# Optimization experiments

Measured on AMD Instinct MI355X. Metric: run time of the kernel, lower is better.

Reference implementation:

```python
import jax, jax.numpy as jnp
import numpy as np


def _gcn_layer(x, src, dst, W, b):
    """PyG GCNConv: out = D^-1/2 (A+I) D^-1/2 (x @ W) + b, symmetric norm with self-loops."""
    n = x.shape[0]
    h = x @ W  # [n, out]
    loop = jnp.arange(n, dtype=src.dtype)
    s = jnp.concatenate([src, loop])  # self-loops appended
    d = jnp.concatenate([dst, loop])
    deg = jax.ops.segment_sum(jnp.ones_like(s, dtype=x.dtype), d, num_segments=n)
    dinv = jax.lax.rsqrt(jnp.maximum(deg, 1.0))  # deg >= 1 due to self-loops
    coef = dinv[s] * dinv[d]  # [E+n]
    agg = jax.ops.segment_sum(h[s] * coef[:, None], d, num_segments=n)  # [n, out]
    return agg + b


def setup_inputs() -> dict:
    key = jax.random.key(0)
    k = jax.random.split(key, 6)
    N, E, IN, HID, OUT = 100000, 3200000, 256, 256, 128
    x = jax.random.normal(k[0], (N, IN), dtype=jnp.float32)
    edge_index = jax.random.randint(k[1], (2, E), 0, N, dtype=jnp.int64)
    # Glorot-ish init for weights, zero bias (PyG defaults)
    W1 = jax.random.normal(k[2], (IN, HID), dtype=jnp.float32) * (1.0 / np.sqrt(IN))
    b1 = jnp.zeros((HID,), dtype=jnp.float32)
    W2 = jax.random.normal(k[3], (HID, OUT), dtype=jnp.float32) * (1.0 / np.sqrt(HID))
    b2 = jnp.zeros((OUT,), dtype=jnp.float32)
    return {"x": x, "edge_index": edge_index, "W1": W1, "b1": b1, "W2": W2, "b2": b2}


def reference(x, edge_index, W1, b1, W2, b2):
    src, dst = edge_index[0], edge_index[1]
    h = jax.nn.relu(_gcn_layer(x, src, dst, W1, b1))
    return _gcn_layer(h, src, dst, W2, b2)
```

## Files before the change

kernel.cpp:

```cpp
#include <hip/hip_runtime.h>

using f32x4 = __attribute__((ext_vector_type(4))) float;
using s16x8 = __attribute__((ext_vector_type(8))) short;

static __device__ __forceinline__ unsigned short f2bf(float f) {
    union { float f; unsigned u; } v; v.f = f;
    unsigned r = v.u + 0x7fffu + ((v.u >> 16) & 1u);
    return (unsigned short)(r >> 16);
}
static __device__ __forceinline__ float bf2f(unsigned short h) {
    union { unsigned u; float f; } v; v.u = ((unsigned)h) << 16;
    return v.f;
}


__global__ __launch_bounds__(256) void partition_edges256(
        const int* __restrict__ src, const int* __restrict__ dst,
        int2* __restrict__ qpair, int* __restrict__ qcnt,
        int E, int span2, int qcap) {
    __shared__ int2 buf[256][32];
    __shared__ int cnt[256];
    const int tid = threadIdx.x;
    cnt[tid] = 0;
    __syncthreads();

    const int e0 = blockIdx.x * 2048;
    const int e1 = min(e0 + 2048, E);
    for (int i = e0 + tid; i < e1; i += 256) {
        int d = dst[i];
        int s = src[i];
        int b = (unsigned)d / (unsigned)span2;
        int p = atomicAdd(&cnt[b], 1);
        if (p < 32) {
            buf[b][p] = make_int2(d, s);
        } else {
            int gp = atomicAdd(&qcnt[b], 1);
            qpair[(size_t)b * qcap + gp] = make_int2(d, s);
        }
    }
    __syncthreads();
    int c = min(cnt[tid], 32);
    if (c > 0) {
        int gb = atomicAdd(&qcnt[tid], c);
        int2* q = qpair + (size_t)tid * qcap + gb;
        for (int j = 0; j < c; ++j) q[j] = buf[tid][j];
    }
}


__global__ __launch_bounds__(1024) void hist_bucket(
        const int2* __restrict__ qpair, const int* __restrict__ qcnt,
        int* __restrict__ deg, int N, int span2, int qcap) {
    __shared__ int h[512];
    const int b = blockIdx.x;
    const int base = b * span2;
    for (int k = threadIdx.x; k < span2; k += 1024) h[k] = 0;
    __syncthreads();
    const int len = qcnt[b];
    const int2* q = qpair + (size_t)b * qcap;
    for (int i = threadIdx.x; i < len; i += 1024)
        atomicAdd(&h[q[i].x - base], 1);
    __syncthreads();
    int width = N - base; if (width > span2) width = span2; if (width < 0) width = 0;
    for (int k = threadIdx.x; k < width; k += 1024) deg[base + k] = h[k];
}


__global__ void scan_blocks(const int* __restrict__ deg, int* __restrict__ excl,
                            int* __restrict__ block_sums, float* __restrict__ dinv, int n) {
    __shared__ int s[256];
    int t = threadIdx.x;
    int gid = blockIdx.x * 256 + t;
    int v = (gid < n) ? deg[gid] : 0;
    if (gid < n) dinv[gid] = rsqrtf((float)(v + 1));
    s[t] = v;
    __syncthreads();
    #pragma unroll
    for (int off = 1; off < 256; off <<= 1) {
        int add = (t >= off) ? s[t - off] : 0;
        __syncthreads();
        s[t] += add;
        __syncthreads();
    }
    if (gid < n) excl[gid] = s[t] - v;
    if (t == 255) block_sums[blockIdx.x] = s[255];
}

__global__ void scan_sums(int* __restrict__ block_sums, int nb) {
    __shared__ int s[512];
    int t = threadIdx.x;
    int v = (t < nb) ? block_sums[t] : 0;
    s[t] = v;
    __syncthreads();
    #pragma unroll
    for (int off = 1; off < 512; off <<= 1) {
        int add = (t >= off) ? s[t - off] : 0;
        __syncthreads();
        s[t] += add;
        __syncthreads();
    }
    if (t < nb) block_sums[t] = s[t] - v;
}

__global__ void scan_add(int* __restrict__ excl, const int* __restrict__ block_sums,
                         int n, int E) {
    int gid = blockIdx.x * 256 + threadIdx.x;
    if (gid < n) excl[gid] += block_sums[gid >> 8];
    if (gid == n) excl[n] = E;
}


__global__ __launch_bounds__(1024) void place_bucket(
        const int2* __restrict__ qpair, const int* __restrict__ qcnt,
        const int* __restrict__ rp, int* __restrict__ sorted_src,
        int N, int span2, int qcap) {
    __shared__ int cur[512];
    const int b = blockIdx.x;
    const int base = b * span2;
    for (int k = threadIdx.x; k < span2; k += 1024) {
        int idx = base + k;
        cur[k] = (idx < N) ? rp[idx] : 0;
    }
    __syncthreads();
    const int len = qcnt[b];
    const int2* q = qpair + (size_t)b * qcap;
    for (int i = threadIdx.x; i < len; i += 1024) {
        int2 p = q[i];
        int pos = atomicAdd(&cur[p.x - base], 1);
        sorted_src[pos] = p.y;
    }
}


__global__ void convert_weights_t(const float* __restrict__ W1, const float* __restrict__ W2,
                                  unsigned short* __restrict__ W1t, unsigned short* __restrict__ W2t,
                                  int K, int N1, int N2) {
    int i = blockIdx.x * blockDim.x + threadIdx.x;
    int k4 = K / 4;
    int tot1 = N1 * k4;
    int tot2 = N2 * k4;
    if (i < tot1) {
        int n = i / k4, k0 = (i % k4) * 4;
        ushort4 o = make_ushort4(f2bf(W1[(size_t)(k0 + 0) * N1 + n]),
                                 f2bf(W1[(size_t)(k0 + 1) * N1 + n]),
                                 f2bf(W1[(size_t)(k0 + 2) * N1 + n]),
                                 f2bf(W1[(size_t)(k0 + 3) * N1 + n]));
        *(ushort4*)&W1t[(size_t)n * K + k0] = o;
    } else if (i - tot1 < tot2) {
        int j = i - tot1;
        int n = j / k4, k0 = (j % k4) * 4;
        ushort4 o = make_ushort4(f2bf(W2[(size_t)(k0 + 0) * N2 + n]),
                                 f2bf(W2[(size_t)(k0 + 1) * N2 + n]),
                                 f2bf(W2[(size_t)(k0 + 2) * N2 + n]),
                                 f2bf(W2[(size_t)(k0 + 3) * N2 + n]));
        *(ushort4*)&W2t[(size_t)n * K + k0] = o;
    }
}


template<int BN, bool AF32>
__global__ __launch_bounds__(512) void gemm_mfma(
        const void* __restrict__ Av, const unsigned short* __restrict__ Bt_g,
        unsigned short* __restrict__ C, const float* __restrict__ dinv,
        int M, int K) {
    constexpr int FN = BN / 64;
    __shared__ __align__(16) short As[128][40];
    __shared__ __align__(16) short Bt[BN][40];

    const int tid  = threadIdx.x;
    const int lane = tid & 63;
    const int wave = tid >> 6;
    const int wm = wave >> 2;
    const int wn = wave & 3;
    const int brow = blockIdx.x * 128;

    const int fr = lane & 15;
    const int kk = (lane >> 4) * 8;

    const int ar = tid >> 2;
    const int ac = (tid & 3) * 8;

    f32x4 acc[4][FN] = {};

    for (int k0 = 0; k0 < K; k0 += 32) {
        {
            int gr = brow + ar;
            s16x8 s = {};
            if (gr < M) {
                if constexpr (AF32) {
                    const float* A = (const float*)Av;
                    float4 v0 = *(const float4*)&A[(size_t)gr * K + k0 + ac];
                    float4 v1 = *(const float4*)&A[(size_t)gr * K + k0 + ac + 4];
                    s[0] = (short)f2bf(v0.x); s[1] = (short)f2bf(v0.y);
                    s[2] = (short)f2bf(v0.z); s[3] = (short)f2bf(v0.w);
                    s[4] = (short)f2bf(v1.x); s[5] = (short)f2bf(v1.y);
                    s[6] = (short)f2bf(v1.z); s[7] = (short)f2bf(v1.w);
                } else {
                    const unsigned short* A = (const unsigned short*)Av;
                    s = *(const s16x8*)&A[(size_t)gr * K + k0 + ac];
                }
            }
            *(s16x8*)&As[ar][ac] = s;
        }
        #pragma unroll
        for (int p = 0; p < BN / 128; ++p) {
            int ci = tid + p * 512;
            int col = ci >> 2;
            int kc = (ci & 3) * 8;
            s16x8 v = *(const s16x8*)&Bt_g[(size_t)col * K + k0 + kc];
            *(s16x8*)&Bt[col][kc] = v;
        }
        __syncthreads();

        s16x8 af[4], bv[FN];
        #pragma unroll
        for (int fm = 0; fm < 4; ++fm)
            af[fm] = *(const s16x8*)&As[wm * 64 + fm * 16 + fr][kk];
        #pragma unroll
        for (int fn = 0; fn < FN; ++fn)
            bv[fn] = *(const s16x8*)&Bt[wn * (BN / 4) + fn * 16 + fr][kk];
        #pragma unroll
        for (int fm = 0; fm < 4; ++fm)
            #pragma unroll
            for (int fn = 0; fn < FN; ++fn)
                acc[fm][fn] = __builtin_amdgcn_mfma_f32_16x16x32_bf16(
                    af[fm], bv[fn], acc[fm][fn], 0, 0, 0);
        __syncthreads();
    }

    const int orow = (lane >> 4) * 4;
    #pragma unroll
    for (int fm = 0; fm < 4; ++fm) {
        #pragma unroll
        for (int reg = 0; reg < 4; ++reg) {
            int gr = brow + wm * 64 + fm * 16 + orow + reg;
            if (gr < M) {
                float dv = dinv[gr];
                #pragma unroll
                for (int fn = 0; fn < FN; ++fn) {
                    int gc = wn * (BN / 4) + fn * 16 + fr;
                    C[(size_t)gr * BN + gc] = f2bf(dv * acc[fm][fn][reg]);
                }
            }
        }
    }
}


__global__ __launch_bounds__(256) void agg_pull_256_bf16(
        const int* __restrict__ rp, const int* __restrict__ sorted_src,
        const float* __restrict__ dinv, const unsigned short* __restrict__ Hs,
        const float* __restrict__ bias, unsigned short* __restrict__ outb, int N) {
    int node = blockIdx.x * 4 + (threadIdx.x >> 6);
    int lane = threadIdx.x & 63;
    if (node >= N) return;

    int r0 = rp[node];
    int r1 = rp[node + 1];
    int c = lane << 2;
    ushort4 hv = *(const ushort4*)&Hs[(size_t)node * 256 + c];
    float a0 = bf2f(hv.x), a1 = bf2f(hv.y), a2 = bf2f(hv.z), a3 = bf2f(hv.w);

    int i = r0;
    for (; i + 8 <= r1; i += 8) {
        int s[8];
        #pragma unroll
        for (int u = 0; u < 8; ++u) s[u] = sorted_src[i + u];
        ushort4 h[8];
        #pragma unroll
        for (int u = 0; u < 8; ++u) h[u] = *(const ushort4*)&Hs[(size_t)s[u] * 256 + c];
        #pragma unroll
        for (int u = 0; u < 8; ++u) {
            a0 += bf2f(h[u].x); a1 += bf2f(h[u].y);
            a2 += bf2f(h[u].z); a3 += bf2f(h[u].w);
        }
    }
    if (i + 4 <= r1) {
        int s[4];
        #pragma unroll
        for (int u = 0; u < 4; ++u) s[u] = sorted_src[i + u];
        ushort4 h[4];
        #pragma unroll
        for (int u = 0; u < 4; ++u) h[u] = *(const ushort4*)&Hs[(size_t)s[u] * 256 + c];
        #pragma unroll
        for (int u = 0; u < 4; ++u) {
            a0 += bf2f(h[u].x); a1 += bf2f(h[u].y);
            a2 += bf2f(h[u].z); a3 += bf2f(h[u].w);
        }
        i += 4;
    }
    for (; i < r1; ++i) {
        ushort4 h = *(const ushort4*)&Hs[(size_t)sorted_src[i] * 256 + c];
        a0 += bf2f(h.x); a1 += bf2f(h.y); a2 += bf2f(h.z); a3 += bf2f(h.w);
    }

    float dv = dinv[node];
    float4 bb = *(const float4*)&bias[c];
    float o0 = fmaxf(bb.x + dv * a0, 0.f);
    float o1 = fmaxf(bb.y + dv * a1, 0.f);
    float o2 = fmaxf(bb.z + dv * a2, 0.f);
    float o3 = fmaxf(bb.w + dv * a3, 0.f);
    *(ushort4*)&outb[(size_t)node * 256 + c] = make_ushort4(f2bf(o0), f2bf(o1), f2bf(o2), f2bf(o3));
}


__global__ __launch_bounds__(256) void agg_pull_128_bf16(
        const int* __restrict__ rp, const int* __restrict__ sorted_src,
        const float* __restrict__ dinv, const unsigned short* __restrict__ Hs,
        const float* __restrict__ bias, float* __restrict__ out, int N) {
    int node = blockIdx.x * 8 + ((threadIdx.x >> 6) << 1) + ((threadIdx.x >> 5) & 1);
    int l = threadIdx.x & 31;
    if (node >= N) return;

    int r0 = rp[node];
    int r1 = rp[node + 1];
    int c = l << 2;
    ushort4 hv = *(const ushort4*)&Hs[(size_t)node * 128 + c];
    float a0 = bf2f(hv.x), a1 = bf2f(hv.y), a2 = bf2f(hv.z), a3 = bf2f(hv.w);

    int i = r0;
    for (; i + 8 <= r1; i += 8) {
        int s[8];
        #pragma unroll
        for (int u = 0; u < 8; ++u) s[u] = sorted_src[i + u];
        ushort4 h[8];
        #pragma unroll
        for (int u = 0; u < 8; ++u) h[u] = *(const ushort4*)&Hs[(size_t)s[u] * 128 + c];
        #pragma unroll
        for (int u = 0; u < 8; ++u) {
            a0 += bf2f(h[u].x); a1 += bf2f(h[u].y);
            a2 += bf2f(h[u].z); a3 += bf2f(h[u].w);
        }
    }
    if (i + 4 <= r1) {
        int s[4];
        #pragma unroll
        for (int u = 0; u < 4; ++u) s[u] = sorted_src[i + u];
        ushort4 h[4];
        #pragma unroll
        for (int u = 0; u < 4; ++u) h[u] = *(const ushort4*)&Hs[(size_t)s[u] * 128 + c];
        #pragma unroll
        for (int u = 0; u < 4; ++u) {
            a0 += bf2f(h[u].x); a1 += bf2f(h[u].y);
            a2 += bf2f(h[u].z); a3 += bf2f(h[u].w);
        }
        i += 4;
    }
    for (; i < r1; ++i) {
        ushort4 h = *(const ushort4*)&Hs[(size_t)sorted_src[i] * 128 + c];
        a0 += bf2f(h.x); a1 += bf2f(h.y); a2 += bf2f(h.z); a3 += bf2f(h.w);
    }

    float dv = dinv[node];
    float4 bb = *(const float4*)&bias[c];
    float4 o = make_float4(bb.x + dv * a0, bb.y + dv * a1,
                           bb.z + dv * a2, bb.w + dv * a3);
    *(float4*)&out[(size_t)node * 128 + c] = o;
}


extern "C" void kernel_launch(void* const* d_in, const int* in_sizes, int n_in,
                              void* d_out, int out_size, void* d_ws, size_t ws_size,
                              hipStream_t stream) {
    const float* x   = (const float*)d_in[0];
    const int*   ei  = (const int*)d_in[1];
    const float* W1  = (const float*)d_in[2];
    const float* b1  = (const float*)d_in[3];
    const float* W2  = (const float*)d_in[4];
    const float* b2  = (const float*)d_in[5];
    float* out       = (float*)d_out;

    const int E   = in_sizes[1] / 2;
    const int HID = in_sizes[3];
    const int IN  = in_sizes[2] / HID;
    const int OUT = in_sizes[5];
    const int N   = in_sizes[0] / IN;
    const int span2 = (N + 255) / 256;
    const int qcap  = E / 256 + 1536;

    char* ws = (char*)d_ws;
    int*   row_ptr    = (int*)ws;
    int*   deg        = (int*)(ws + (512 << 10));
    float* dinv       = (float*)(ws + (1 << 20));
    int*   block_sums = (int*)(ws + 1572864);
    int*   qcnt       = (int*)(ws + 1638400);
    unsigned short* W1t = (unsigned short*)(ws + 1703936);
    unsigned short* W2t = (unsigned short*)(ws + 1867776);
    int*   sorted_src = (int*)(ws + (2 << 20));
    unsigned short* Hsb = (unsigned short*)(ws + ((size_t)16 << 20));
    unsigned short* A1b = (unsigned short*)(ws + ((size_t)80 << 20));
    int2*  qpair      = (int2*)(ws + ((size_t)136 << 20));

    const int* e_src = ei;
    const int* e_dst = ei + E;
    const int nb_scan = (N + 255) / 256;

    hipMemsetAsync(qcnt, 0, 256 * sizeof(int), stream);
    partition_edges256<<<(E + 2047) / 2048, 256, 0, stream>>>(e_src, e_dst, qpair, qcnt,
                                                              E, span2, qcap);
    hist_bucket<<<256, 1024, 0, stream>>>(qpair, qcnt, deg, N, span2, qcap);
    scan_blocks<<<nb_scan, 256, 0, stream>>>(deg, row_ptr, block_sums, dinv, N);
    scan_sums<<<1, 512, 0, stream>>>(block_sums, nb_scan);
    scan_add<<<(N + 256) / 256, 256, 0, stream>>>(row_ptr, block_sums, N, E);
    place_bucket<<<256, 1024, 0, stream>>>(qpair, qcnt, row_ptr, sorted_src, N, span2, qcap);

    convert_weights_t<<<96, 256, 0, stream>>>(W1, W2, W1t, W2t, IN, HID, OUT);

    gemm_mfma<256, true><<<(N + 127) / 128, 512, 0, stream>>>(x, W1t, Hsb, dinv, N, IN);
    agg_pull_256_bf16<<<(N + 3) / 4, 256, 0, stream>>>(row_ptr, sorted_src, dinv, Hsb, b1, A1b, N);

    gemm_mfma<128, false><<<(N + 127) / 128, 512, 0, stream>>>(A1b, W2t, Hsb, dinv, N, HID);
    agg_pull_128_bf16<<<(N + 7) / 8, 256, 0, stream>>>(row_ptr, sorted_src, dinv, Hsb, b2, out, N);
}
```

Baseline: 485.7 us.

## Fuse CSR build into one bucket kernel and prefetch GEMM A tiles into registers

Merges the histogram, the three-pass prefix scan and the placement kernel into a single per-bucket kernel. Each bucket finds its global edge offset by summing the earlier bucket counts and scans its own 512 node degrees locally, which removes four launches and the deg/block_sums round trips through global memory. The GEMM now loads the next K-slice of A into registers while the current slice is computed, and gets a launch-bounds occupancy hint. The in-block scan assumes span2 <= 512, and the extra prefetch registers could lower occupancy.

```diff
diff --git a/kernel.cpp b/kernel.cpp
--- a/kernel.cpp
+++ b/kernel.cpp
@@ -48,85 +48,53 @@
 }
 
 
-__global__ __launch_bounds__(1024) void hist_bucket(
+__global__ __launch_bounds__(1024) void csr_bucket(
         const int2* __restrict__ qpair, const int* __restrict__ qcnt,
-        int* __restrict__ deg, int N, int span2, int qcap) {
+        int* __restrict__ row_ptr, float* __restrict__ dinv,
+        int* __restrict__ sorted_src, int N, int E, int span2, int qcap) {
+    __shared__ int red[256];
     __shared__ int h[512];
     const int b = blockIdx.x;
     const int base = b * span2;
-    for (int k = threadIdx.x; k < span2; k += 1024) h[k] = 0;
-    __syncthreads();
+    const int tid = threadIdx.x;
+
+    if (tid < 256) red[tid] = (tid < b) ? qcnt[tid] : 0;
+    __syncthreads();
+    #pragma unroll
+    for (int off = 128; off > 0; off >>= 1) {
+        if (tid < off) red[tid] += red[tid + off];
+        __syncthreads();
+    }
+    const int qbase = red[0];
     const int len = qcnt[b];
     const int2* q = qpair + (size_t)b * qcap;
-    for (int i = threadIdx.x; i < len; i += 1024)
+
+    if (tid < 512) h[tid] = 0;
+    __syncthreads();
+    for (int i = tid; i < len; i += 1024)
         atomicAdd(&h[q[i].x - base], 1);
     __syncthreads();
-    int width = N - base; if (width > span2) width = span2; if (width < 0) width = 0;
-    for (int k = threadIdx.x; k < width; k += 1024) deg[base + k] = h[k];
-}
-
-
-__global__ void scan_blocks(const int* __restrict__ deg, int* __restrict__ excl,
-                            int* __restrict__ block_sums, float* __restrict__ dinv, int n) {
-    __shared__ int s[256];
-    int t = threadIdx.x;
-    int gid = blockIdx.x * 256 + t;
-    int v = (gid < n) ? deg[gid] : 0;
-    if (gid < n) dinv[gid] = rsqrtf((float)(v + 1));
-    s[t] = v;
-    __syncthreads();
-    #pragma unroll
-    for (int off = 1; off < 256; off <<= 1) {
-        int add = (t >= off) ? s[t - off] : 0;
-        __syncthreads();
-        s[t] += add;
-        __syncthreads();
-    }
-    if (gid < n) excl[gid] = s[t] - v;
-    if (t == 255) block_sums[blockIdx.x] = s[255];
-}
-
-__global__ void scan_sums(int* __restrict__ block_sums, int nb) {
-    __shared__ int s[512];
-    int t = threadIdx.x;
-    int v = (t < nb) ? block_sums[t] : 0;
-    s[t] = v;
-    __syncthreads();
+
+    int deg_t = (tid < 512) ? h[tid] : 0;
     #pragma unroll
     for (int off = 1; off < 512; off <<= 1) {
-        int add = (t >= off) ? s[t - off] : 0;
-        __syncthreads();
-        s[t] += add;
-        __syncthreads();
-    }
-    if (t < nb) block_sums[t] = s[t] - v;
-}
-
-__global__ void scan_add(int* __restrict__ excl, const int* __restrict__ block_sums,
-                         int n, int E) {
-    int gid = blockIdx.x * 256 + threadIdx.x;
-    if (gid < n) excl[gid] += block_sums[gid >> 8];
-    if (gid == n) excl[n] = E;
-}
-
-
-__global__ __launch_bounds__(1024) void place_bucket(
-        const int2* __restrict__ qpair, const int* __restrict__ qcnt,
-        const int* __restrict__ rp, int* __restrict__ sorted_src,
-        int N, int span2, int qcap) {
-    __shared__ int cur[512];
-    const int b = blockIdx.x;
-    const int base = b * span2;
-    for (int k = threadIdx.x; k < span2; k += 1024) {
-        int idx = base + k;
-        cur[k] = (idx < N) ? rp[idx] : 0;
-    }
-    __syncthreads();
-    const int len = qcnt[b];
-    const int2* q = qpair + (size_t)b * qcap;
-    for (int i = threadIdx.x; i < len; i += 1024) {
+        int add = (tid >= off && tid < 512) ? h[tid - off] : 0;
+        __syncthreads();
+        if (tid < 512) h[tid] += add;
+        __syncthreads();
+    }
+    int width = N - base; if (width > span2) width = span2; if (width < 0) width = 0;
+    if (tid < width) {
+        row_ptr[base + tid] = qbase + h[tid] - deg_t;
+        dinv[base + tid] = rsqrtf((float)(deg_t + 1));
+    }
+    if (b == 255 && tid == 0) row_ptr[N] = E;
+
+    if (tid < 512) h[tid] = qbase + h[tid] - deg_t;
+    __syncthreads();
+    for (int i = tid; i < len; i += 1024) {
         int2 p = q[i];
-        int pos = atomicAdd(&cur[p.x - base], 1);
+        int pos = atomicAdd(&h[p.x - base], 1);
         sorted_src[pos] = p.y;
     }
 }
@@ -159,7 +127,7 @@
 
 
 template<int BN, bool AF32>
-__global__ __launch_bounds__(512) void gemm_mfma(
+__global__ __launch_bounds__(512, 4) void gemm_mfma(
         const void* __restrict__ Av, const unsigned short* __restrict__ Bt_g,
         unsigned short* __restrict__ C, const float* __restrict__ dinv,
         int M, int K) {
@@ -179,26 +147,33 @@
 
     const int ar = tid >> 2;
     const int ac = (tid & 3) * 8;
+    const int gr = brow + ar;
 
     f32x4 acc[4][FN] = {};
+    float4 pa0 = make_float4(0.f, 0.f, 0.f, 0.f), pa1 = pa0;
+    s16x8 pas = {};
+
+    if (gr < M) {
+        if constexpr (AF32) {
+            const float* A = (const float*)Av;
+            pa0 = *(const float4*)&A[(size_t)gr * K + ac];
+            pa1 = *(const float4*)&A[(size_t)gr * K + ac + 4];
+        } else {
+            const unsigned short* A = (const unsigned short*)Av;
+            pas = *(const s16x8*)&A[(size_t)gr * K + ac];
+        }
+    }
 
     for (int k0 = 0; k0 < K; k0 += 32) {
         {
-            int gr = brow + ar;
-            s16x8 s = {};
-            if (gr < M) {
-                if constexpr (AF32) {
-                    const float* A = (const float*)Av;
-                    float4 v0 = *(const float4*)&A[(size_t)gr * K + k0 + ac];
-                    float4 v1 = *(const float4*)&A[(size_t)gr * K + k0 + ac + 4];
-                    s[0] = (short)f2bf(v0.x); s[1] = (short)f2bf(v0.y);
-                    s[2] = (short)f2bf(v0.z); s[3] = (short)f2bf(v0.w);
-                    s[4] = (short)f2bf(v1.x); s[5] = (short)f2bf(v1.y);
-                    s[6] = (short)f2bf(v1.z); s[7] = (short)f2bf(v1.w);
-                } else {
-                    const unsigned short* A = (const unsigned short*)Av;
-                    s = *(const s16x8*)&A[(size_t)gr * K + k0 + ac];
-                }
+            s16x8 s;
+            if constexpr (AF32) {
+                s[0] = (short)f2bf(pa0.x); s[1] = (short)f2bf(pa0.y);
+                s[2] = (short)f2bf(pa0.z); s[3] = (short)f2bf(pa0.w);
+                s[4] = (short)f2bf(pa1.x); s[5] = (short)f2bf(pa1.y);
+                s[6] = (short)f2bf(pa1.z); s[7] = (short)f2bf(pa1.w);
+            } else {
+                s = pas;
             }
             *(s16x8*)&As[ar][ac] = s;
         }
@@ -207,10 +182,21 @@
             int ci = tid + p * 512;
             int col = ci >> 2;
             int kc = (ci & 3) * 8;
-            s16x8 v = *(const s16x8*)&Bt_g[(size_t)col * K + k0 + kc];
-            *(s16x8*)&Bt[col][kc] = v;
-        }
-        __syncthreads();
+            *(s16x8*)&Bt[col][kc] = *(const s16x8*)&Bt_g[(size_t)col * K + k0 + kc];
+        }
+        __syncthreads();
+
+        int kn = k0 + 32;
+        if (kn < K && gr < M) {
+            if constexpr (AF32) {
+                const float* A = (const float*)Av;
+                pa0 = *(const float4*)&A[(size_t)gr * K + kn + ac];
+                pa1 = *(const float4*)&A[(size_t)gr * K + kn + ac + 4];
+            } else {
+                const unsigned short* A = (const unsigned short*)Av;
+                pas = *(const s16x8*)&A[(size_t)gr * K + kn + ac];
+            }
+        }
 
         s16x8 af[4], bv[FN];
         #pragma unroll
@@ -233,13 +219,13 @@
     for (int fm = 0; fm < 4; ++fm) {
         #pragma unroll
         for (int reg = 0; reg < 4; ++reg) {
-            int gr = brow + wm * 64 + fm * 16 + orow + reg;
-            if (gr < M) {
-                float dv = dinv[gr];
+            int grr = brow + wm * 64 + fm * 16 + orow + reg;
+            if (grr < M) {
+                float dv = dinv[grr];
                 #pragma unroll
                 for (int fn = 0; fn < FN; ++fn) {
                     int gc = wn * (BN / 4) + fn * 16 + fr;
-                    C[(size_t)gr * BN + gc] = f2bf(dv * acc[fm][fn][reg]);
+                    C[(size_t)grr * BN + gc] = f2bf(dv * acc[fm][fn][reg]);
                 }
             }
         }
@@ -380,9 +366,7 @@
 
     char* ws = (char*)d_ws;
     int*   row_ptr    = (int*)ws;
-    int*   deg        = (int*)(ws + (512 << 10));
     float* dinv       = (float*)(ws + (1 << 20));
-    int*   block_sums = (int*)(ws + 1572864);
     int*   qcnt       = (int*)(ws + 1638400);
     unsigned short* W1t = (unsigned short*)(ws + 1703936);
     unsigned short* W2t = (unsigned short*)(ws + 1867776);
@@ -393,16 +377,12 @@
 
     const int* e_src = ei;
     const int* e_dst = ei + E;
-    const int nb_scan = (N + 255) / 256;
 
     hipMemsetAsync(qcnt, 0, 256 * sizeof(int), stream);
     partition_edges256<<<(E + 2047) / 2048, 256, 0, stream>>>(e_src, e_dst, qpair, qcnt,
                                                               E, span2, qcap);
-    hist_bucket<<<256, 1024, 0, stream>>>(qpair, qcnt, deg, N, span2, qcap);
-    scan_blocks<<<nb_scan, 256, 0, stream>>>(deg, row_ptr, block_sums, dinv, N);
-    scan_sums<<<1, 512, 0, stream>>>(block_sums, nb_scan);
-    scan_add<<<(N + 256) / 256, 256, 0, stream>>>(row_ptr, block_sums, N, E);
-    place_bucket<<<256, 1024, 0, stream>>>(qpair, qcnt, row_ptr, sorted_src, N, span2, qcap);
+    csr_bucket<<<256, 1024, 0, stream>>>(qpair, qcnt, row_ptr, dinv, sorted_src,
+                                         N, E, span2, qcap);
 
     convert_weights_t<<<96, 256, 0, stream>>>(W1, W2, W1t, W2t, IN, HID, OUT);
 
```

Measured after the change: 475.3 us. 2.1% less time.
